# Optimization experiments

Hardware: AMD Instinct MI355X
Metric: run time of the kernel (lower is better)

## Reference

```python
import jax, jax.numpy as jnp
import numpy as np

B = 4        # number of point clouds (equal-sized, batch ids are sorted blocks)
K = 3        # knn_interpolate k
EPS_D = 1e-16
EPS_BN = 1e-5


def setup_inputs() -> dict:
    key = jax.random.key(0)
    ks = jax.random.split(key, 12)
    N_src, N_tgt = 2048, 8192
    C, C_skip = 256, 128
    x = jax.random.normal(ks[0], (B * N_src, C), dtype=jnp.float32)
    pos = jax.random.normal(ks[1], (B * N_src, 3), dtype=jnp.float32)
    x_skip = jax.random.normal(ks[2], (B * N_tgt, C_skip), dtype=jnp.float32)
    pos_skip = jax.random.normal(ks[3], (B * N_tgt, 3), dtype=jnp.float32)
    batch = jnp.repeat(jnp.arange(B, dtype=jnp.int64), N_src)
    batch_skip = jnp.repeat(jnp.arange(B, dtype=jnp.int64), N_tgt)
    d_in = C + C_skip  # 384
    W1 = jax.random.normal(ks[4], (d_in, 256), dtype=jnp.float32) / np.sqrt(d_in)
    b1 = jnp.zeros((256,), dtype=jnp.float32)
    g1 = jnp.ones((256,), dtype=jnp.float32)
    be1 = jnp.zeros((256,), dtype=jnp.float32)
    W2 = jax.random.normal(ks[5], (256, 256), dtype=jnp.float32) / 16.0
    b2 = jnp.zeros((256,), dtype=jnp.float32)
    g2 = jnp.ones((256,), dtype=jnp.float32)
    be2 = jnp.zeros((256,), dtype=jnp.float32)
    return dict(x=x, pos=pos, batch=batch, x_skip=x_skip, pos_skip=pos_skip,
                batch_skip=batch_skip, W1=W1, b1=b1, g1=g1, be1=be1,
                W2=W2, b2=b2, g2=g2, be2=be2)


def _knn_interpolate(x, pos, pos_skip):
    # equal-size clouds: reshape instead of per-batch masking
    C = x.shape[1]
    N = pos.shape[0] // B
    M = pos_skip.shape[0] // B
    ps = pos.reshape(B, N, 3)
    pt = pos_skip.reshape(B, M, 3)
    # squared distances [B, M, N] via |a|^2 + |b|^2 - 2ab
    d2 = (jnp.sum(pt * pt, -1)[:, :, None]
          + jnp.sum(ps * ps, -1)[:, None, :]
          - 2.0 * jnp.einsum('bmd,bnd->bmn', pt, ps))
    neg_d2, idx = jax.lax.top_k(-d2, K)            # idx: [B, M, K]
    w = 1.0 / jnp.maximum(-neg_d2, EPS_D)          # inverse squared distance
    xf = x.reshape(B, N, C)
    feats = xf[jnp.arange(B)[:, None, None], idx]  # [B, M, K, C] irregular gather
    y = jnp.sum(feats * w[..., None], axis=2) / jnp.sum(w, axis=2)[..., None]
    return y.reshape(B * M, C)


def _mlp_block(h, W, b, g, be):
    h = jnp.maximum(h @ W + b, 0.0)                # Linear + ReLU
    mu = jnp.mean(h, axis=0)
    var = jnp.mean((h - mu) ** 2, axis=0)          # biased var (torch BN training)
    return g * (h - mu) / jnp.sqrt(var + EPS_BN) + be


def reference(x, pos, batch, x_skip, pos_skip, batch_skip,
              W1, b1, g1, be1, W2, b2, g2, be2):
    y = _knn_interpolate(x, pos, pos_skip)
    h = jnp.concatenate([y, x_skip], axis=1)       # [B*M, 384]
    h = _mlp_block(h, W1, b1, g1, be1)
    h = _mlp_block(h, W2, b2, g2, be2)
    return h
```

## Files before the change

### kernel.cpp

```cpp
#include <hip/hip_runtime.h>
#include <hip/hip_bf16.h>

typedef __attribute__((ext_vector_type(8))) short short8;
typedef __attribute__((ext_vector_type(4))) float f32x4;
typedef __attribute__((ext_vector_type(2))) float f32x2;
typedef __attribute__((ext_vector_type(8))) float f32x8;

constexpr int BATCH  = 4;
constexpr int NSRC   = 2048;
constexpr int NTGT   = 8192;
constexpr int C_IN   = 256;
constexpr int C_SKIP = 128;
constexpr int DIN    = 384;
constexpr int HID    = 256;
constexpr int MROWS  = BATCH * NTGT;

constexpr int TGT_PER_BLK = 16;
constexpr int KNN_BLOCKS  = MROWS / TGT_PER_BLK;
constexpr int WT_BLOCKS   = 8;
constexpr int LDS_STRIDE  = 36;

__global__ __launch_bounds__(512, 4) void knn_h_kernel(const float* __restrict__ pos,
                                                       const float* __restrict__ pos_skip,
                                                       const float* __restrict__ x,
                                                       const float* __restrict__ xs,
                                                       const float* __restrict__ W1,
                                                       __hip_bfloat16* __restrict__ W1T,
                                                       __hip_bfloat16* __restrict__ H0,
                                                       float* __restrict__ stats) {
#pragma clang fp contract(off)
    const int blk = blockIdx.x;
    if (blk >= KNN_BLOCKS) {
        const int e = blk - KNN_BLOCKS;
        if (e < WT_BLOCKS) {
            const int r  = e * 32 + (threadIdx.x >> 4);
            const int c0 = threadIdx.x & 15;
#pragma unroll
            for (int k = 0; k < DIN / 16; ++k) {
                int c = c0 + k * 16;
                W1T[(size_t)r * DIN + c] = __float2bfloat16(W1[(size_t)c * HID + r]);
            }
        } else {
            for (int i = threadIdx.x; i < 4 * HID; i += 512) stats[i] = 0.0f;
        }
        return;
    }
    __shared__ float4 sp[NSRC];
    __shared__ float  sd[TGT_PER_BLK][3];
    __shared__ int    si[TGT_PER_BLK][3];
    const int t0 = blk * TGT_PER_BLK;
    const int b  = t0 / NTGT;
    const float* ps = pos + (size_t)b * NSRC * 3;
    for (int j = threadIdx.x; j < NSRC; j += 512) {
        float X = ps[j * 3 + 0], Y = ps[j * 3 + 1], Z = ps[j * 3 + 2];
        float s2 = ((X * X) + (Y * Y)) + (Z * Z);
        sp[j] = make_float4(X, Y, Z, s2);
    }
    __syncthreads();
    const int g  = threadIdx.x >> 5;
    const int s  = threadIdx.x & 31;
    const int tr = t0 + g;
    const float px = pos_skip[tr * 3 + 0], py = pos_skip[tr * 3 + 1], pz = pos_skip[tr * 3 + 2];
    const float pt2 = ((px * px) + (py * py)) + (pz * pz);
    const f32x2 px2 = {px, px}, py2 = {py, py}, pz2 = {pz, pz}, ptv = {pt2, pt2};
    float bd0 = 3e38f, bd1 = 3e38f, bd2 = 3e38f;
    int   bi0 = 0x7fffffff, bi1 = 0x7fffffff, bi2 = 0x7fffffff;
#pragma unroll 4
    for (int k = 0; k < NSRC / 64; ++k) {
        const int j1 = k * 64 + s;
        const int j2 = j1 + 32;
        float4 sa = sp[j1];
        float4 sb = sp[j2];
        f32x2 vx = {sa.x, sb.x}, vy = {sa.y, sb.y}, vz = {sa.z, sb.z}, vw = {sa.w, sb.w};
        f32x2 dot = ((px2 * vx) + (py2 * vy)) + (pz2 * vz);
        f32x2 d2v = (ptv + vw) - (f32x2{2.0f, 2.0f} * dot);
#pragma unroll
        for (int h = 0; h < 2; ++h) {
            float d2 = h == 0 ? d2v.x : d2v.y;
            int   j  = h == 0 ? j1 : j2;
            bool c0 = d2 < bd0, c1 = d2 < bd1, c2 = d2 < bd2;
            bd2 = c1 ? bd1 : (c2 ? d2 : bd2);  bi2 = c1 ? bi1 : (c2 ? j : bi2);
            bd1 = c0 ? bd0 : (c1 ? d2 : bd1);  bi1 = c0 ? bi0 : (c1 ? j : bi1);
            bd0 = c0 ? d2  : bd0;              bi0 = c0 ? j  : bi0;
        }
    }
#pragma unroll
    for (int m = 1; m <= 16; m <<= 1) {
        float od0 = __shfl_xor(bd0, m), od1 = __shfl_xor(bd1, m), od2 = __shfl_xor(bd2, m);
        int   oi0 = __shfl_xor(bi0, m), oi1 = __shfl_xor(bi1, m), oi2 = __shfl_xor(bi2, m);
#pragma unroll
        for (int e = 0; e < 3; ++e) {
            float d = e == 0 ? od0 : (e == 1 ? od1 : od2);
            int   i = e == 0 ? oi0 : (e == 1 ? oi1 : oi2);
            bool c0 = (d < bd0) || (d == bd0 && i < bi0);
            bool c1 = (d < bd1) || (d == bd1 && i < bi1);
            bool c2 = (d < bd2) || (d == bd2 && i < bi2);
            bd2 = c1 ? bd1 : (c2 ? d : bd2);  bi2 = c1 ? bi1 : (c2 ? i : bi2);
            bd1 = c0 ? bd0 : (c1 ? d : bd1);  bi1 = c0 ? bi0 : (c1 ? i : bi1);
            bd0 = c0 ? d   : bd0;             bi0 = c0 ? i  : bi0;
        }
    }
    if (s == 0) {
        sd[g][0] = bd0; sd[g][1] = bd1; sd[g][2] = bd2;
        si[g][0] = bi0; si[g][1] = bi1; si[g][2] = bi2;
    }
    __syncthreads();
    const int w = threadIdx.x >> 6, lane = threadIdx.x & 63;
    const float* xb = x + (size_t)b * NSRC * C_IN;
#pragma unroll
    for (int u = 0; u < 2; ++u) {
        const int tt = w * 2 + u;
        const int r  = t0 + tt;
        float w0 = 1.0f / fmaxf(sd[tt][0], 1e-16f);
        float w1 = 1.0f / fmaxf(sd[tt][1], 1e-16f);
        float w2 = 1.0f / fmaxf(sd[tt][2], 1e-16f);
        float inv = 1.0f / ((w0 + w1) + w2);
        const float* f0 = xb + (size_t)si[tt][0] * C_IN;
        const float* f1 = xb + (size_t)si[tt][1] * C_IN;
        const float* f2 = xb + (size_t)si[tt][2] * C_IN;
        __hip_bfloat16* o = H0 + (size_t)r * DIN;
#pragma unroll
        for (int kk = 0; kk < 4; ++kk) {
            int c = lane + kk * 64;
            float v = ((w0 * f0[c] + w1 * f1[c]) + w2 * f2[c]) * inv;
            o[c] = __float2bfloat16(v);
        }
        const float* srow = xs + (size_t)r * C_SKIP;
#pragma unroll
        for (int kk = 0; kk < 2; ++kk) {
            int c = lane + kk * 64;
            o[C_IN + c] = __float2bfloat16(srow[c]);
        }
    }
}

template <int K>
__global__ __launch_bounds__(256, 1) void gemm_kernel(const __hip_bfloat16* __restrict__ A,
                                                      const __hip_bfloat16* __restrict__ WT,
                                                      const float* __restrict__ bias,
                                                      __hip_bfloat16* __restrict__ outp,
                                                      float* __restrict__ colsum,
                                                      float* __restrict__ colsq) {
    __shared__ short As[128 * LDS_STRIDE];
    const int t = threadIdx.x;
    const int m0 = blockIdx.x * 128;
    const int wid = t >> 6, lane = t & 63;
    const int wr = wid & 1, wcq = wid >> 1;
    const int l15 = lane & 15, l4 = lane >> 4;
    const int arow = t >> 1, acol8 = (t & 1) * 8;
    f32x4 acc[4][8] = {};
    const short* Ash = (const short*)A;
    const short* Wsh = (const short*)WT;
    for (int kt = 0; kt < K / 32; ++kt) {
        short8 v0 = *(const short8*)(Ash + (size_t)(m0 + arow) * K + kt * 32 + acol8);
        short8 v1 = *(const short8*)(Ash + (size_t)(m0 + arow) * K + kt * 32 + acol8 + 16);
        __syncthreads();
        *(short8*)(&As[arow * LDS_STRIDE + acol8]) = v0;
        *(short8*)(&As[arow * LDS_STRIDE + acol8 + 16]) = v1;
        __syncthreads();
        short8 af[4], bfr[8];
#pragma unroll
        for (int mi = 0; mi < 4; ++mi)
            af[mi] = *(const short8*)(&As[(wr * 64 + mi * 16 + l15) * LDS_STRIDE + l4 * 8]);
#pragma unroll
        for (int ni = 0; ni < 8; ++ni)
            bfr[ni] = *(const short8*)(Wsh + (size_t)(wcq * 128 + ni * 16 + l15) * K + kt * 32 + l4 * 8);
#pragma unroll
        for (int mi = 0; mi < 4; ++mi)
#pragma unroll
            for (int ni = 0; ni < 8; ++ni)
                acc[mi][ni] = __builtin_amdgcn_mfma_f32_16x16x32_bf16(af[mi], bfr[ni], acc[mi][ni], 0, 0, 0);
    }
    float bv[8];
    int col[8];
#pragma unroll
    for (int ni = 0; ni < 8; ++ni) {
        col[ni] = wcq * 128 + ni * 16 + l15;
        bv[ni] = bias[col[ni]];
    }
    float csum[8] = {}, csq[8] = {};
#pragma unroll
    for (int mi = 0; mi < 4; ++mi) {
#pragma unroll
        for (int r = 0; r < 4; ++r) {
            int rowg = m0 + wr * 64 + mi * 16 + l4 * 4 + r;
#pragma unroll
            for (int ni = 0; ni < 8; ++ni) {
                float v = fmaxf(acc[mi][ni][r] + bv[ni], 0.0f);
                outp[(size_t)rowg * HID + col[ni]] = __float2bfloat16(v);
                csum[ni] += v;
                csq[ni] += v * v;
            }
        }
    }
#pragma unroll
    for (int ni = 0; ni < 8; ++ni) {
        float sv = csum[ni], q = csq[ni];
        sv += __shfl_xor(sv, 16); sv += __shfl_xor(sv, 32);
        q  += __shfl_xor(q, 16);  q  += __shfl_xor(q, 32);
        if (l4 == 0) {
            atomicAdd(&colsum[col[ni]], sv);
            atomicAdd(&colsq[col[ni]], q);
        }
    }
}

__global__ __launch_bounds__(256) void foldw2_kernel(const float* __restrict__ W2,
                                                     const float* __restrict__ b2,
                                                     const float* __restrict__ sum1,
                                                     const float* __restrict__ sq1,
                                                     const float* __restrict__ g1,
                                                     const float* __restrict__ be1,
                                                     __hip_bfloat16* __restrict__ W2T,
                                                     float* __restrict__ bias2f) {
    __shared__ float red[256];
    const int n = blockIdx.x, k = threadIdx.x;
    float mu  = sum1[k] * (1.0f / MROWS);
    float var = sq1[k] * (1.0f / MROWS) - mu * mu;
    float scv = g1[k] / sqrtf(var + 1e-5f);
    float shv = be1[k] - mu * scv;
    float v = W2[(size_t)k * HID + n];
    W2T[(size_t)n * HID + k] = __float2bfloat16(scv * v);
    red[k] = shv * v;
    __syncthreads();
    for (int s = 128; s > 0; s >>= 1) {
        if (k < s) red[k] += red[k + s];
        __syncthreads();
    }
    if (k == 0) bias2f[n] = b2[n] + red[0];
}

__global__ __launch_bounds__(256) void bn2_kernel(const __hip_bfloat16* __restrict__ h2,
                                                  const float* __restrict__ sum2,
                                                  const float* __restrict__ sq2,
                                                  const float* __restrict__ g2,
                                                  const float* __restrict__ be2,
                                                  float* __restrict__ out) {
    __shared__ float lsc[HID], lsh[HID];
    {
        int c = threadIdx.x;
        float mu  = sum2[c] * (1.0f / MROWS);
        float var = sq2[c] * (1.0f / MROWS) - mu * mu;
        float scv = g2[c] / sqrtf(var + 1e-5f);
        lsc[c] = scv;
        lsh[c] = be2[c] - mu * scv;
    }
    __syncthreads();
    int idx = blockIdx.x * blockDim.x + threadIdx.x;
    const int total = MROWS * HID / 8;
    for (; idx < total; idx += gridDim.x * blockDim.x) {
        short8 v = *(const short8*)(h2 + (size_t)idx * 8);
        int c = (idx * 8) & (HID - 1);
        f32x8 o;
#pragma unroll
        for (int e = 0; e < 8; ++e) {
            float f = __uint_as_float(((unsigned)(unsigned short)v[e]) << 16);
            o[e] = lsc[c + e] * f + lsh[c + e];
        }
        *(f32x8*)(out + (size_t)idx * 8) = o;
    }
}

extern "C" void kernel_launch(void* const* d_in, const int* in_sizes, int n_in,
                              void* d_out, int out_size, void* d_ws, size_t ws_size,
                              hipStream_t stream) {
    const float* x    = (const float*)d_in[0];
    const float* pos  = (const float*)d_in[1];
    const float* xs   = (const float*)d_in[3];
    const float* poss = (const float*)d_in[4];
    const float* W1   = (const float*)d_in[6];
    const float* b1   = (const float*)d_in[7];
    const float* g1   = (const float*)d_in[8];
    const float* be1  = (const float*)d_in[9];
    const float* W2   = (const float*)d_in[10];
    const float* b2   = (const float*)d_in[11];
    const float* g2   = (const float*)d_in[12];
    const float* be2  = (const float*)d_in[13];

    char* ws = (char*)d_ws;
    size_t off = 0;
    auto alloc = [&](size_t bytes) -> void* {
        void* p = ws + off;
        off += (bytes + 255) & ~(size_t)255;
        return p;
    };
    __hip_bfloat16* W1T   = (__hip_bfloat16*)alloc((size_t)HID * DIN * 2);
    __hip_bfloat16* W2T   = (__hip_bfloat16*)alloc((size_t)HID * HID * 2);
    float*          stats = (float*)alloc(4 * HID * sizeof(float));
    float *sum1 = stats, *sq1 = stats + HID, *sum2 = stats + 2 * HID, *sq2 = stats + 3 * HID;
    float*          bias2f = (float*)alloc(HID * sizeof(float));
    __hip_bfloat16* H0 = (__hip_bfloat16*)alloc((size_t)MROWS * DIN * 2);
    __hip_bfloat16* H1 = (__hip_bfloat16*)alloc((size_t)MROWS * HID * 2);
    __hip_bfloat16* H2 = H0;

    knn_h_kernel<<<KNN_BLOCKS + WT_BLOCKS + 1, 512, 0, stream>>>(pos, poss, x, xs, W1, W1T, H0, stats);
    gemm_kernel<DIN><<<MROWS / 128, 256, 0, stream>>>(H0, W1T, b1, H1, sum1, sq1);
    foldw2_kernel<<<HID, 256, 0, stream>>>(W2, b2, sum1, sq1, g1, be1, W2T, bias2f);
    gemm_kernel<HID><<<MROWS / 128, 256, 0, stream>>>(H1, W2T, bias2f, H2, sum2, sq2);
    bn2_kernel<<<1024, 256, 0, stream>>>(H2, sum2, sq2, g2, be2, (float*)d_out);
}
```

Measured before the change: 136.8 us.

## Use direct global-to-LDS loads with XOR swizzle and smaller GEMM row tiles

The GEMM kernel now stages A tiles with global_load_lds directly into LDS, which removes the register round trip. LDS is laid out with an XOR-swizzled 64-wide K chunk instead of a padded stride. The row tile drops from 128 to 64 and the K step grows to 64, with launch bounds raised to two blocks per CU. This doubles the grid to improve occupancy and wave count across the CUs, at the cost of loading the B (weight) fragments from global memory twice as often per output row.

Measured after the change: 164.6 us. 20.3% more time.

```diff
diff --git a/kernel.cpp b/kernel.cpp
--- a/kernel.cpp
+++ b/kernel.cpp
@@ -18,7 +18,6 @@
 constexpr int TGT_PER_BLK = 16;
 constexpr int KNN_BLOCKS  = MROWS / TGT_PER_BLK;
 constexpr int WT_BLOCKS   = 8;
-constexpr int LDS_STRIDE  = 36;
 
 __global__ __launch_bounds__(512, 4) void knn_h_kernel(const float* __restrict__ pos,
                                                        const float* __restrict__ pos_skip,
@@ -135,41 +134,53 @@
 }
 
 template <int K>
-__global__ __launch_bounds__(256, 1) void gemm_kernel(const __hip_bfloat16* __restrict__ A,
+__global__ __launch_bounds__(256, 2) void gemm_kernel(const __hip_bfloat16* __restrict__ A,
                                                       const __hip_bfloat16* __restrict__ WT,
                                                       const float* __restrict__ bias,
                                                       __hip_bfloat16* __restrict__ outp,
                                                       float* __restrict__ colsum,
                                                       float* __restrict__ colsq) {
-    __shared__ short As[128 * LDS_STRIDE];
+    __shared__ short As[64 * 64];
     const int t = threadIdx.x;
-    const int m0 = blockIdx.x * 128;
+    const int m0 = blockIdx.x * 64;
     const int wid = t >> 6, lane = t & 63;
     const int wr = wid & 1, wcq = wid >> 1;
     const int l15 = lane & 15, l4 = lane >> 4;
-    const int arow = t >> 1, acol8 = (t & 1) * 8;
-    f32x4 acc[4][8] = {};
+    const int srow  = wid * 8 + (lane >> 3);
+    const int schunk = lane & 7;
+    const int scol  = (schunk ^ (srow & 7)) * 8;
     const short* Ash = (const short*)A;
     const short* Wsh = (const short*)WT;
-    for (int kt = 0; kt < K / 32; ++kt) {
-        short8 v0 = *(const short8*)(Ash + (size_t)(m0 + arow) * K + kt * 32 + acol8);
-        short8 v1 = *(const short8*)(Ash + (size_t)(m0 + arow) * K + kt * 32 + acol8 + 16);
+    f32x4 acc[2][8] = {};
+    for (int kt = 0; kt < K / 64; ++kt) {
         __syncthreads();
-        *(short8*)(&As[arow * LDS_STRIDE + acol8]) = v0;
-        *(short8*)(&As[arow * LDS_STRIDE + acol8 + 16]) = v1;
+        __builtin_amdgcn_global_load_lds(
+            (const __attribute__((address_space(1))) void*)(Ash + (size_t)(m0 + srow) * K + kt * 64 + scol),
+            (__attribute__((address_space(3))) void*)(As + wid * 512),
+            16, 0, 0);
+        __builtin_amdgcn_global_load_lds(
+            (const __attribute__((address_space(1))) void*)(Ash + (size_t)(m0 + srow + 32) * K + kt * 64 + scol),
+            (__attribute__((address_space(3))) void*)(As + 2048 + wid * 512),
+            16, 0, 0);
         __syncthreads();
-        short8 af[4], bfr[8];
-#pragma unroll
-        for (int mi = 0; mi < 4; ++mi)
-            af[mi] = *(const short8*)(&As[(wr * 64 + mi * 16 + l15) * LDS_STRIDE + l4 * 8]);
-#pragma unroll
-        for (int ni = 0; ni < 8; ++ni)
-            bfr[ni] = *(const short8*)(Wsh + (size_t)(wcq * 128 + ni * 16 + l15) * K + kt * 32 + l4 * 8);
-#pragma unroll
-        for (int mi = 0; mi < 4; ++mi)
+#pragma unroll
+        for (int kk = 0; kk < 2; ++kk) {
+            short8 af[2], bfr[8];
+#pragma unroll
+            for (int mi = 0; mi < 2; ++mi) {
+                int row = wr * 32 + mi * 16 + l15;
+                int chunk = (kk * 4 + l4) ^ (row & 7);
+                af[mi] = *(const short8*)(&As[row * 64 + chunk * 8]);
+            }
 #pragma unroll
             for (int ni = 0; ni < 8; ++ni)
-                acc[mi][ni] = __builtin_amdgcn_mfma_f32_16x16x32_bf16(af[mi], bfr[ni], acc[mi][ni], 0, 0, 0);
+                bfr[ni] = *(const short8*)(Wsh + (size_t)(wcq * 128 + ni * 16 + l15) * K + kt * 64 + kk * 32 + l4 * 8);
+#pragma unroll
+            for (int mi = 0; mi < 2; ++mi)
+#pragma unroll
+                for (int ni = 0; ni < 8; ++ni)
+                    acc[mi][ni] = __builtin_amdgcn_mfma_f32_16x16x32_bf16(af[mi], bfr[ni], acc[mi][ni], 0, 0, 0);
+        }
     }
     float bv[8];
     int col[8];
@@ -180,10 +191,10 @@
     }
     float csum[8] = {}, csq[8] = {};
 #pragma unroll
-    for (int mi = 0; mi < 4; ++mi) {
+    for (int mi = 0; mi < 2; ++mi) {
 #pragma unroll
         for (int r = 0; r < 4; ++r) {
-            int rowg = m0 + wr * 64 + mi * 16 + l4 * 4 + r;
+            int rowg = m0 + wr * 32 + mi * 16 + l4 * 4 + r;
 #pragma unroll
             for (int ni = 0; ni < 8; ++ni) {
                 float v = fmaxf(acc[mi][ni][r] + bv[ni], 0.0f);
@@ -294,8 +305,8 @@
     __hip_bfloat16* H2 = H0;
 
     knn_h_kernel<<<KNN_BLOCKS + WT_BLOCKS + 1, 512, 0, stream>>>(pos, poss, x, xs, W1, W1T, H0, stats);
-    gemm_kernel<DIN><<<MROWS / 128, 256, 0, stream>>>(H0, W1T, b1, H1, sum1, sq1);
+    gemm_kernel<DIN><<<MROWS / 64, 256, 0, stream>>>(H0, W1T, b1, H1, sum1, sq1);
     foldw2_kernel<<<HID, 256, 0, stream>>>(W2, b2, sum1, sq1, g1, be1, W2T, bias2f);
-    gemm_kernel<HID><<<MROWS / 128, 256, 0, stream>>>(H1, W2T, bias2f, H2, sum2, sq2);
+    gemm_kernel<HID><<<MROWS / 64, 256, 0, stream>>>(H1, W2T, bias2f, H2, sum2, sq2);
     bn2_kernel<<<1024, 256, 0, stream>>>(H2, sum2, sq2, g2, be2, (float*)d_out);
 }
```

## Two-pass kNN: compute top-3 distance threshold, then gated index selection

Applied to the files above, without the earlier changes.

Replaces the single-pass top-3 insertion with index tracking by a first pass that tracks only the three smallest distances with min/med3 ops and a shuffle merge across the wave. A second pass recomputes distances and performs the full index-tracking insertion only when a candidate is within the threshold. This is meant to reduce the per-candidate select instruction count, at the cost of doubling distance computation and LDS reads and adding a divergent branch.

Result: slower. 142.7 us (+4.3%).

```diff
diff --git a/kernel.cpp b/kernel.cpp
--- a/kernel.cpp
+++ b/kernel.cpp
@@ -63,8 +63,9 @@
     const float px = pos_skip[tr * 3 + 0], py = pos_skip[tr * 3 + 1], pz = pos_skip[tr * 3 + 2];
     const float pt2 = ((px * px) + (py * py)) + (pz * pz);
     const f32x2 px2 = {px, px}, py2 = {py, py}, pz2 = {pz, pz}, ptv = {pt2, pt2};
-    float bd0 = 3e38f, bd1 = 3e38f, bd2 = 3e38f;
-    int   bi0 = 0x7fffffff, bi1 = 0x7fffffff, bi2 = 0x7fffffff;
+    const f32x2 two = {2.0f, 2.0f};
+
+    float a0 = 3e38f, a1 = 3e38f, a2 = 3e38f;
 #pragma unroll 4
     for (int k = 0; k < NSRC / 64; ++k) {
         const int j1 = k * 64 + s;
@@ -73,15 +74,48 @@
         float4 sb = sp[j2];
         f32x2 vx = {sa.x, sb.x}, vy = {sa.y, sb.y}, vz = {sa.z, sb.z}, vw = {sa.w, sb.w};
         f32x2 dot = ((px2 * vx) + (py2 * vy)) + (pz2 * vz);
-        f32x2 d2v = (ptv + vw) - (f32x2{2.0f, 2.0f} * dot);
+        f32x2 d2v = (ptv + vw) - (two * dot);
 #pragma unroll
         for (int h = 0; h < 2; ++h) {
-            float d2 = h == 0 ? d2v.x : d2v.y;
-            int   j  = h == 0 ? j1 : j2;
-            bool c0 = d2 < bd0, c1 = d2 < bd1, c2 = d2 < bd2;
-            bd2 = c1 ? bd1 : (c2 ? d2 : bd2);  bi2 = c1 ? bi1 : (c2 ? j : bi2);
-            bd1 = c0 ? bd0 : (c1 ? d2 : bd1);  bi1 = c0 ? bi0 : (c1 ? j : bi1);
-            bd0 = c0 ? d2  : bd0;              bi0 = c0 ? j  : bi0;
+            float d = h == 0 ? d2v.x : d2v.y;
+            float n0 = fminf(a0, d);
+            float n1 = __builtin_amdgcn_fmed3f(a0, a1, d);
+            float n2 = fminf(a2, fmaxf(a1, d));
+            a0 = n0; a1 = n1; a2 = n2;
+        }
+    }
+#pragma unroll
+    for (int m = 1; m <= 16; m <<= 1) {
+        float oa = __shfl_xor(a0, m), ob = __shfl_xor(a1, m), oc = __shfl_xor(a2, m);
+        float minb = fminf(a1, ob), maxb = fmaxf(a1, ob);
+        float mina = fminf(a0, oa), maxa = fmaxf(a0, oa);
+        float minc = fminf(a2, oc);
+        float n0 = mina;
+        float n1 = __builtin_amdgcn_fmed3f(a0, oa, minb);
+        float n2 = __builtin_amdgcn_fmed3f(minb, maxa, fminf(maxb, minc));
+        a0 = n0; a1 = n1; a2 = n2;
+    }
+
+    float bd0 = 3e38f, bd1 = 3e38f, bd2 = 3e38f;
+    int   bi0 = 0x7fffffff, bi1 = 0x7fffffff, bi2 = 0x7fffffff;
+    for (int k = 0; k < NSRC / 64; ++k) {
+        const int j1 = k * 64 + s;
+        const int j2 = j1 + 32;
+        float4 sa = sp[j1];
+        float4 sb = sp[j2];
+        f32x2 vx = {sa.x, sb.x}, vy = {sa.y, sb.y}, vz = {sa.z, sb.z}, vw = {sa.w, sb.w};
+        f32x2 dot = ((px2 * vx) + (py2 * vy)) + (pz2 * vz);
+        f32x2 d2v = (ptv + vw) - (two * dot);
+        if (d2v.x <= a2 || d2v.y <= a2) {
+#pragma unroll
+            for (int h = 0; h < 2; ++h) {
+                float d2 = h == 0 ? d2v.x : d2v.y;
+                int   j  = h == 0 ? j1 : j2;
+                bool c0 = d2 < bd0, c1 = d2 < bd1, c2 = d2 < bd2;
+                bd2 = c1 ? bd1 : (c2 ? d2 : bd2);  bi2 = c1 ? bi1 : (c2 ? j : bi2);
+                bd1 = c0 ? bd0 : (c1 ? d2 : bd1);  bi1 = c0 ? bi0 : (c1 ? j : bi1);
+                bd0 = c0 ? d2  : bd0;              bi0 = c0 ? j  : bi0;
+            }
         }
     }
 #pragma unroll
```

## Apply first linear layer before KNN interpolation to shrink the first GEMM

Applied to the files above, without the earlier changes.

Uses linearity to project the source features x through W1's top rows once per source point (8192 rows) and the skip features through the bottom rows, then interpolates the projected rows using the stored KNN indices and weights. The KNN kernel now only writes indices and normalized weights, and a new interp kernel fuses the weighted gather, skip add, bias, ReLU and BN1 statistics. This removes the 32768x384 GEMM input and the H0 buffer, replacing it with a smaller projection plus a gather, but it rounds the projected values to bf16 before interpolation and adds an extra launch.

Result: slower. 179.6 us (+31.2%).

```diff
diff --git a/kernel.cpp b/kernel.cpp
--- a/kernel.cpp
+++ b/kernel.cpp
@@ -2,6 +2,8 @@
 #include <hip/hip_bf16.h>
 
 typedef __attribute__((ext_vector_type(8))) short short8;
+typedef __attribute__((ext_vector_type(4))) short s16x4;
+typedef __attribute__((ext_vector_type(4))) int   i32x4;
 typedef __attribute__((ext_vector_type(4))) float f32x4;
 typedef __attribute__((ext_vector_type(2))) float f32x2;
 typedef __attribute__((ext_vector_type(8))) float f32x8;
@@ -20,14 +22,21 @@
 constexpr int WT_BLOCKS   = 8;
 constexpr int LDS_STRIDE  = 36;
 
-__global__ __launch_bounds__(512, 4) void knn_h_kernel(const float* __restrict__ pos,
-                                                       const float* __restrict__ pos_skip,
-                                                       const float* __restrict__ x,
-                                                       const float* __restrict__ xs,
-                                                       const float* __restrict__ W1,
-                                                       __hip_bfloat16* __restrict__ W1T,
-                                                       __hip_bfloat16* __restrict__ H0,
-                                                       float* __restrict__ stats) {
+__device__ __forceinline__ short f2bf(float v) {
+    __hip_bfloat16 h = __float2bfloat16(v);
+    return (short)__builtin_bit_cast(unsigned short, h);
+}
+__device__ __forceinline__ float bf2f(short s) {
+    return __uint_as_float(((unsigned)(unsigned short)s) << 16);
+}
+
+__global__ __launch_bounds__(512, 4) void knn_kernel(const float* __restrict__ pos,
+                                                     const float* __restrict__ pos_skip,
+                                                     const float* __restrict__ W1,
+                                                     __hip_bfloat16* __restrict__ W1T,
+                                                     i32x4* __restrict__ idxo,
+                                                     f32x4* __restrict__ wqo,
+                                                     float* __restrict__ stats) {
 #pragma clang fp contract(off)
     const int blk = blockIdx.x;
     if (blk >= KNN_BLOCKS) {
@@ -46,8 +55,6 @@
         return;
     }
     __shared__ float4 sp[NSRC];
-    __shared__ float  sd[TGT_PER_BLK][3];
-    __shared__ int    si[TGT_PER_BLK][3];
     const int t0 = blk * TGT_PER_BLK;
     const int b  = t0 / NTGT;
     const float* ps = pos + (size_t)b * NSRC * 3;
@@ -63,6 +70,7 @@
     const float px = pos_skip[tr * 3 + 0], py = pos_skip[tr * 3 + 1], pz = pos_skip[tr * 3 + 2];
     const float pt2 = ((px * px) + (py * py)) + (pz * pz);
     const f32x2 px2 = {px, px}, py2 = {py, py}, pz2 = {pz, pz}, ptv = {pt2, pt2};
+    const f32x2 two = {2.0f, 2.0f};
     float bd0 = 3e38f, bd1 = 3e38f, bd2 = 3e38f;
     int   bi0 = 0x7fffffff, bi1 = 0x7fffffff, bi2 = 0x7fffffff;
 #pragma unroll 4
@@ -73,7 +81,7 @@
         float4 sb = sp[j2];
         f32x2 vx = {sa.x, sb.x}, vy = {sa.y, sb.y}, vz = {sa.z, sb.z}, vw = {sa.w, sb.w};
         f32x2 dot = ((px2 * vx) + (py2 * vy)) + (pz2 * vz);
-        f32x2 d2v = (ptv + vw) - (f32x2{2.0f, 2.0f} * dot);
+        f32x2 d2v = (ptv + vw) - (two * dot);
 #pragma unroll
         for (int h = 0; h < 2; ++h) {
             float d2 = h == 0 ? d2v.x : d2v.y;
@@ -101,35 +109,121 @@
         }
     }
     if (s == 0) {
-        sd[g][0] = bd0; sd[g][1] = bd1; sd[g][2] = bd2;
-        si[g][0] = bi0; si[g][1] = bi1; si[g][2] = bi2;
-    }
+        float w0 = 1.0f / fmaxf(bd0, 1e-16f);
+        float w1 = 1.0f / fmaxf(bd1, 1e-16f);
+        float w2 = 1.0f / fmaxf(bd2, 1e-16f);
+        float inv = 1.0f / ((w0 + w1) + w2);
+        idxo[tr] = i32x4{bi0, bi1, bi2, 0};
+        wqo[tr]  = f32x4{w0 * inv, w1 * inv, w2 * inv, 0.0f};
+    }
+}
+
+__global__ __launch_bounds__(256, 1) void zs_kernel(const float* __restrict__ x,
+                                                    const float* __restrict__ xs,
+                                                    const __hip_bfloat16* __restrict__ W1T,
+                                                    __hip_bfloat16* __restrict__ Z,
+                                                    __hip_bfloat16* __restrict__ S) {
+    __shared__ short As[128 * LDS_STRIDE];
+    const int blk = blockIdx.x;
+    const float* A;
+    __hip_bfloat16* out;
+    int K, koff, m0;
+    if (blk < 64) { A = x;  out = Z; K = 256; koff = 0;   m0 = blk * 128; }
+    else          { A = xs; out = S; K = 128; koff = 256; m0 = (blk - 64) * 128; }
+    const int t = threadIdx.x;
+    const int wid = t >> 6, lane = t & 63;
+    const int wr = wid & 1, wcq = wid >> 1;
+    const int l15 = lane & 15, l4 = lane >> 4;
+    const int arow = t >> 1, ac16 = (t & 1) * 16;
+    const short* Wsh = (const short*)W1T;
+    f32x4 acc[4][8] = {};
+    for (int kt = 0; kt < K / 32; ++kt) {
+        const float* src = A + (size_t)(m0 + arow) * K + kt * 32 + ac16;
+        float4 f0 = *(const float4*)(src);
+        float4 f1 = *(const float4*)(src + 4);
+        float4 f2 = *(const float4*)(src + 8);
+        float4 f3 = *(const float4*)(src + 12);
+        short8 s0 = {f2bf(f0.x), f2bf(f0.y), f2bf(f0.z), f2bf(f0.w),
+                     f2bf(f1.x), f2bf(f1.y), f2bf(f1.z), f2bf(f1.w)};
+        short8 s1 = {f2bf(f2.x), f2bf(f2.y), f2bf(f2.z), f2bf(f2.w),
+                     f2bf(f3.x), f2bf(f3.y), f2bf(f3.z), f2bf(f3.w)};
+        __syncthreads();
+        *(short8*)(&As[arow * LDS_STRIDE + ac16])     = s0;
+        *(short8*)(&As[arow * LDS_STRIDE + ac16 + 8]) = s1;
+        __syncthreads();
+        short8 af[4], bfr[8];
+#pragma unroll
+        for (int mi = 0; mi < 4; ++mi)
+            af[mi] = *(const short8*)(&As[(wr * 64 + mi * 16 + l15) * LDS_STRIDE + l4 * 8]);
+#pragma unroll
+        for (int ni = 0; ni < 8; ++ni)
+            bfr[ni] = *(const short8*)(Wsh + (size_t)(wcq * 128 + ni * 16 + l15) * DIN + koff + kt * 32 + l4 * 8);
+#pragma unroll
+        for (int mi = 0; mi < 4; ++mi)
+#pragma unroll
+            for (int ni = 0; ni < 8; ++ni)
+                acc[mi][ni] = __builtin_amdgcn_mfma_f32_16x16x32_bf16(af[mi], bfr[ni], acc[mi][ni], 0, 0, 0);
+    }
+#pragma unroll
+    for (int mi = 0; mi < 4; ++mi)
+#pragma unroll
+        for (int r = 0; r < 4; ++r) {
+            int rowg = m0 + wr * 64 + mi * 16 + l4 * 4 + r;
+#pragma unroll
+            for (int ni = 0; ni < 8; ++ni) {
+                int col = wcq * 128 + ni * 16 + l15;
+                out[(size_t)rowg * HID + col] = __float2bfloat16(acc[mi][ni][r]);
+            }
+        }
+}
+
+__global__ __launch_bounds__(256) void interp_kernel(const __hip_bfloat16* __restrict__ Z,
+                                                     const __hip_bfloat16* __restrict__ S,
+                                                     const i32x4* __restrict__ idxo,
+                                                     const f32x4* __restrict__ wqo,
+                                                     const float* __restrict__ b1,
+                                                     __hip_bfloat16* __restrict__ H1,
+                                                     float* __restrict__ sum1,
+                                                     float* __restrict__ sq1) {
+    __shared__ float ls[4][HID], lq[4][HID];
+    const int w = threadIdx.x >> 6, lane = threadIdx.x & 63;
+    const int c = lane * 4;
+    f32x4 b1v = *(const f32x4*)(b1 + c);
+    float csum[4] = {}, csq[4] = {};
+    const short* Zs = (const short*)Z;
+    const short* Ss = (const short*)S;
+#pragma unroll 4
+    for (int pass = 0; pass < 16; ++pass) {
+        const int r = blockIdx.x * 64 + pass * 4 + w;
+        i32x4 id = idxo[r];
+        f32x4 wq = wqo[r];
+        const int zb = (r >> 13) << 11;
+        s16x4 z0 = *(const s16x4*)(Zs + (size_t)(zb + id.x) * HID + c);
+        s16x4 z1 = *(const s16x4*)(Zs + (size_t)(zb + id.y) * HID + c);
+        s16x4 z2 = *(const s16x4*)(Zs + (size_t)(zb + id.z) * HID + c);
+        s16x4 sv = *(const s16x4*)(Ss + (size_t)r * HID + c);
+        s16x4 ho;
+#pragma unroll
+        for (int e = 0; e < 4; ++e) {
+            float v = wq.x * bf2f(z0[e]) + wq.y * bf2f(z1[e]) + wq.z * bf2f(z2[e])
+                      + bf2f(sv[e]) + b1v[e];
+            v = fmaxf(v, 0.0f);
+            ho[e] = f2bf(v);
+            csum[e] += v;
+            csq[e] += v * v;
+        }
+        *(s16x4*)((short*)H1 + (size_t)r * HID + c) = ho;
+    }
+    *(f32x4*)(&ls[w][c]) = f32x4{csum[0], csum[1], csum[2], csum[3]};
+    *(f32x4*)(&lq[w][c]) = f32x4{csq[0], csq[1], csq[2], csq[3]};
     __syncthreads();
-    const int w = threadIdx.x >> 6, lane = threadIdx.x & 63;
-    const float* xb = x + (size_t)b * NSRC * C_IN;
-#pragma unroll
-    for (int u = 0; u < 2; ++u) {
-        const int tt = w * 2 + u;
-        const int r  = t0 + tt;
-        float w0 = 1.0f / fmaxf(sd[tt][0], 1e-16f);
-        float w1 = 1.0f / fmaxf(sd[tt][1], 1e-16f);
-        float w2 = 1.0f / fmaxf(sd[tt][2], 1e-16f);
-        float inv = 1.0f / ((w0 + w1) + w2);
-        const float* f0 = xb + (size_t)si[tt][0] * C_IN;
-        const float* f1 = xb + (size_t)si[tt][1] * C_IN;
-        const float* f2 = xb + (size_t)si[tt][2] * C_IN;
-        __hip_bfloat16* o = H0 + (size_t)r * DIN;
-#pragma unroll
-        for (int kk = 0; kk < 4; ++kk) {
-            int c = lane + kk * 64;
-            float v = ((w0 * f0[c] + w1 * f1[c]) + w2 * f2[c]) * inv;
-            o[c] = __float2bfloat16(v);
-        }
-        const float* srow = xs + (size_t)r * C_SKIP;
-#pragma unroll
-        for (int kk = 0; kk < 2; ++kk) {
-            int c = lane + kk * 64;
-            o[C_IN + c] = __float2bfloat16(srow[c]);
+    if (w == 0) {
+#pragma unroll
+        for (int e = 0; e < 4; ++e) {
+            float s_ = ls[0][c + e] + ls[1][c + e] + ls[2][c + e] + ls[3][c + e];
+            float q_ = lq[0][c + e] + lq[1][c + e] + lq[2][c + e] + lq[3][c + e];
+            atomicAdd(&sum1[c + e], s_);
+            atomicAdd(&sq1[c + e], q_);
         }
     }
 }
@@ -254,7 +348,7 @@
         f32x8 o;
 #pragma unroll
         for (int e = 0; e < 8; ++e) {
-            float f = __uint_as_float(((unsigned)(unsigned short)v[e]) << 16);
+            float f = bf2f(v[e]);
             o[e] = lsc[c + e] * f + lsh[c + e];
         }
         *(f32x8*)(out + (size_t)idx * 8) = o;
@@ -289,12 +383,16 @@
     float*          stats = (float*)alloc(4 * HID * sizeof(float));
     float *sum1 = stats, *sq1 = stats + HID, *sum2 = stats + 2 * HID, *sq2 = stats + 3 * HID;
     float*          bias2f = (float*)alloc(HID * sizeof(float));
-    __hip_bfloat16* H0 = (__hip_bfloat16*)alloc((size_t)MROWS * DIN * 2);
-    __hip_bfloat16* H1 = (__hip_bfloat16*)alloc((size_t)MROWS * HID * 2);
-    __hip_bfloat16* H2 = H0;
-
-    knn_h_kernel<<<KNN_BLOCKS + WT_BLOCKS + 1, 512, 0, stream>>>(pos, poss, x, xs, W1, W1T, H0, stats);
-    gemm_kernel<DIN><<<MROWS / 128, 256, 0, stream>>>(H0, W1T, b1, H1, sum1, sq1);
+    i32x4*          idxo  = (i32x4*)alloc((size_t)MROWS * 16);
+    f32x4*          wqo   = (f32x4*)alloc((size_t)MROWS * 16);
+    __hip_bfloat16* Z     = (__hip_bfloat16*)alloc((size_t)BATCH * NSRC * HID * 2);
+    __hip_bfloat16* S     = (__hip_bfloat16*)alloc((size_t)MROWS * HID * 2);
+    __hip_bfloat16* H1    = (__hip_bfloat16*)alloc((size_t)MROWS * HID * 2);
+    __hip_bfloat16* H2    = S;
+
+    knn_kernel<<<KNN_BLOCKS + WT_BLOCKS + 1, 512, 0, stream>>>(pos, poss, W1, W1T, idxo, wqo, stats);
+    zs_kernel<<<64 + MROWS / 128, 256, 0, stream>>>(x, xs, W1T, Z, S);
+    interp_kernel<<<MROWS / 64, 256, 0, stream>>>(Z, S, idxo, wqo, b1, H1, sum1, sq1);
     foldw2_kernel<<<HID, 256, 0, stream>>>(W2, b2, sum1, sq1, g1, be1, W2T, bias2f);
     gemm_kernel<HID><<<MROWS / 128, 256, 0, stream>>>(H1, W2T, bias2f, H2, sum2, sq2);
     bn2_kernel<<<1024, 256, 0, stream>>>(H2, sum2, sq2, g2, be2, (float*)d_out);
```
